# Kernel optimization log

Measured on AMD Instinct MI355X. Metric: run time of the kernel, lower is better.

The kernel has to match this reference:

```python
import jax, jax.numpy as jnp
import numpy as np

B, T, H = 1, 1024, 1024
F2, F3 = 2 * H, 3 * H          # routed / shared ffn dims
S, E, K, R = 8, 32, 4, 64      # shared experts, routed experts, top-k, router rank
EPS = 1e-6


def _rms(x, w):
    # RMSNorm: x * rsqrt(mean(x^2) + eps) * weight
    return x * jax.lax.rsqrt(jnp.mean(x * x, axis=-1, keepdims=True) + EPS) * w


def setup_inputs() -> dict:
    key = jax.random.key(0)
    ks = jax.random.split(key, 10)
    s = 0.02
    return {
        "x": jax.random.normal(ks[0], (B, T, H), dtype=jnp.float32),
        "sn": jnp.ones((S, H), dtype=jnp.float32),                       # shared RMSNorm weights
        "sw1": jax.random.normal(ks[1], (S, H, F3), dtype=jnp.float32) * s,
        "sw2": jax.random.normal(ks[2], (S, F3, H), dtype=jnp.float32) * s,
        "sw3": jax.random.normal(ks[3], (S, H, F3), dtype=jnp.float32) * s,
        "rw1": jax.random.normal(ks[4], (E, H, F2), dtype=jnp.float32) * s,
        "rw2": jax.random.normal(ks[5], (E, F2, H), dtype=jnp.float32) * s,
        "rw3": jax.random.normal(ks[6], (E, H, F2), dtype=jnp.float32) * s,
        "rd": jax.random.normal(ks[7], (H, R), dtype=jnp.float32) * s,   # router_down
        "ru": jax.random.normal(ks[8], (R, E), dtype=jnp.float32) * s,   # router_up
    }


def reference(x, sn, sw1, sw2, sw3, rw1, rw2, rw3, rd, ru):
    b, t, h = x.shape
    xf = x.reshape(-1, h)                                   # [Tk, H]

    # ---- shared experts (AdvancedExpert: RMSNorm + SwiGLU + residual), averaged ----
    xn = _rms(xf[None], sn[:, None, :])                     # [S, Tk, H]
    g = jax.nn.silu(jnp.einsum('sth,shf->stf', xn, sw1))
    v = jnp.einsum('sth,shf->stf', xn, sw3)
    ff = jnp.einsum('stf,sfh->sth', g * v, sw2)             # [S, Tk, H]
    shared = jnp.mean(ff, axis=0) + xf                      # residual averages to +xf

    # ---- router: low-rank logits, top-k, softmax over selected ----
    logits = (xf @ rd) @ ru                                 # [Tk, E]
    rweights, sel = jax.lax.top_k(logits, K)                # [Tk, K]
    rweights = jax.nn.softmax(rweights, axis=-1)
    onehot = jax.nn.one_hot(sel, E, dtype=xf.dtype)         # [Tk, K, E]
    combine = jnp.einsum('tk,tke->te', rweights, onehot)    # [Tk, E]

    # ---- routed experts (Expert: SwiGLU, no norm/residual), weighted combine ----
    g = jax.nn.silu(jnp.einsum('th,ehf->etf', xf, rw1))     # [E, Tk, F2]
    v = jnp.einsum('th,ehf->etf', xf, rw3)
    eouts = jnp.einsum('etf,efh->eth', g * v, rw2)          # [E, Tk, H]
    routed = jnp.einsum('eth,te->th', eouts, combine)

    out = (shared + routed).reshape(b, t, h)

    # ---- aux: load-balance loss = variance (unbiased, like torch .var()) of expert counts ----
    counts = jnp.sum(jax.nn.one_hot(sel.reshape(-1), E, dtype=jnp.float32), axis=0)
    load_balance_loss = jnp.var(counts, ddof=1)
    return out, load_balance_loss
```

## Files before the change

### kernel.cpp

```cpp
#include <hip/hip_runtime.h>
#include <hip/hip_bf16.h>
#include <math.h>

#define TK 1024
#define HD 1024
#define NF3 3072
#define NF2 2048
#define NSH 8
#define NEX 32
#define KSEL 4
#define RRK 64

typedef short bf16x8 __attribute__((ext_vector_type(8)));
typedef float f32x4 __attribute__((ext_vector_type(4)));
typedef unsigned short u16;

__device__ __forceinline__ u16 f2b(float f){
  union{float f; unsigned u;} c; c.f=f;
  unsigned r = c.u + 0x7FFFu + ((c.u>>16)&1u);
  return (u16)(r>>16);
}

__device__ __forceinline__ unsigned pk2(float a, float b){
  __hip_bfloat162 h = __float22bfloat162_rn(float2{a, b});
  union{__hip_bfloat162 h; unsigned u;} c; c.h = h; return c.u;
}

__device__ __forceinline__ int swz8(int row, int c){
  return row*128 + ((c ^ (row&7))<<4);
}

__device__ __forceinline__ int scrofs(int k, int nq){
  return k*256 + (((nq&8) | ((nq&7)^(k&7)))<<4);
}
__device__ __forceinline__ int chunkperm(int c, int k){
  return (c&8) | ((c&7)^(k&7));
}

#define GLDS16(gptr, lptr) \
  __builtin_amdgcn_global_load_lds((const __attribute__((address_space(1))) unsigned*)(gptr), \
                                   (__attribute__((address_space(3))) unsigned*)(lptr), 16, 0, 0)


__global__ void init_kernel(int* counts, int* cursors){
  int i = threadIdx.x;
  if (i < NEX){ counts[i]=0; cursors[i]=0; }
}

__global__ void rms_kernel(const float* __restrict__ x, const float* __restrict__ sn,
                           u16* __restrict__ xb, u16* __restrict__ xnb,
                           float* __restrict__ out, float* __restrict__ rvec, int writeXnb)
{
  const int t = blockIdx.x, tid = threadIdx.x;
  const float4 v = ((const float4*)(x + (size_t)t*HD))[tid];
  float ss = v.x*v.x + v.y*v.y + v.z*v.z + v.w*v.w;
  #pragma unroll
  for (int m=32;m>=1;m>>=1) ss += __shfl_xor(ss, m);
  __shared__ float red[4];
  if ((tid&63)==0) red[tid>>6]=ss;
  __syncthreads();
  const float r = rsqrtf((red[0]+red[1]+red[2]+red[3])*(1.0f/HD) + 1e-6f);
  if (tid==0) rvec[t] = r;
  ushort4 o; o.x=f2b(v.x); o.y=f2b(v.y); o.z=f2b(v.z); o.w=f2b(v.w);
  ((ushort4*)(xb + (size_t)t*HD))[tid] = o;
  if (writeXnb){
    ((float4*)(out + (size_t)t*HD))[tid] = v;
    #pragma unroll
    for (int s=0;s<NSH;s++){
      const float4 g = ((const float4*)(sn + (size_t)s*HD))[tid];
      ushort4 q;
      q.x=f2b(v.x*r*g.x); q.y=f2b(v.y*r*g.y); q.z=f2b(v.z*r*g.z); q.w=f2b(v.w*r*g.w);
      ((ushort4*)(xnb + ((size_t)s*TK + t)*HD))[tid] = q;
    }
  }
}

__global__ void router_kernel(const float* __restrict__ x, const float* __restrict__ rd,
                              const float* __restrict__ ru,
                              int* __restrict__ sel, float* __restrict__ wts,
                              int* __restrict__ counts)
{
  const int t = blockIdx.x, l = threadIdx.x;
  __shared__ float xl[HD];
  __shared__ float xr[RRK];
  __shared__ float lg[NEX];
  const float* xrow = x + (size_t)t*HD;
  for (int i=l;i<HD;i+=64) xl[i]=xrow[i];
  __syncthreads();
  float acc=0.f;
  for (int h=0;h<HD;h++) acc += xl[h]*rd[h*RRK + l];
  xr[l]=acc;
  __syncthreads();
  if (l < NEX){
    float a=0.f;
    for (int r=0;r<RRK;r++) a += xr[r]*ru[r*NEX + l];
    lg[l]=a;
  }
  __syncthreads();
  if (l==0){
    int   sk[KSEL]; float val[KSEL]; unsigned used=0;
    for (int k=0;k<KSEL;k++){
      float best=-1e30f; int bi=0;
      for (int e=0;e<NEX;e++){
        if (used & (1u<<e)) continue;
        if (lg[e] > best){ best=lg[e]; bi=e; }
      }
      used |= (1u<<bi); sk[k]=bi; val[k]=best;
    }
    const float m = val[0];
    float w[KSEL], s=0.f;
    for (int k=0;k<KSEL;k++){ w[k]=expf(val[k]-m); s+=w[k]; }
    for (int k=0;k<KSEL;k++){
      sel[t*KSEL+k]=sk[k]; wts[t*KSEL+k]=w[k]/s;
      atomicAdd(&counts[sk[k]], 1);
    }
  }
}

__global__ void scan_loss_kernel(const int* __restrict__ counts, int* __restrict__ offsets,
                                 float* __restrict__ out_loss)
{
  if (threadIdx.x==0){
    int off=0; float var=0.f;
    for (int e=0;e<NEX;e++){
      offsets[e]=off; off+=counts[e];
      float d = (float)counts[e] - 128.0f;
      var += d*d;
    }
    out_loss[0] = var * (1.0f/31.0f);
  }
}

__global__ void scatter_kernel(const int* __restrict__ sel, const float* __restrict__ wts,
                               const int* __restrict__ offsets, int* __restrict__ cursors,
                               int* __restrict__ tok_of, float* __restrict__ wt_of,
                               int* __restrict__ slot_of)
{
  const int id = blockIdx.x*256 + threadIdx.x;
  const int e = sel[id];
  const int pos = atomicAdd(&cursors[e], 1);
  const int slot = offsets[e] + pos;
  tok_of[slot] = id >> 2;
  wt_of[slot]  = wts[id];
  slot_of[id]  = slot;
}

template<bool SN>
__global__ __launch_bounds__(256) void convT_kernel(const float* __restrict__ src,
                                                    u16* __restrict__ dst, int K, int N,
                                                    const float* __restrict__ sn)
{
  const int z = blockIdx.z;
  const int n0 = blockIdx.x*64, k0 = blockIdx.y*64;
  src += (size_t)z*K*N; dst += (size_t)z*N*K;
  const float* snp = SN ? (sn + (size_t)z*HD + k0) : nullptr;
  __shared__ float tile[64][65];
  const int t = threadIdx.x;
  const int kr = t>>4, nc = t&15;
  #pragma unroll
  for (int i=0;i<4;i++){
    const int k = kr + 16*i;
    const float4 v = *(const float4*)(src + (size_t)(k0+k)*N + n0 + nc*4);
    tile[k][nc*4+0]=v.x; tile[k][nc*4+1]=v.y; tile[k][nc*4+2]=v.z; tile[k][nc*4+3]=v.w;
  }
  __syncthreads();
  const int nr = t>>3, kc = t&7;
  float sv[8];
  #pragma unroll
  for (int j=0;j<8;j++) sv[j] = SN ? snp[kc*8+j] : 1.0f;
  #pragma unroll
  for (int p=0;p<2;p++){
    const int n = nr + 32*p;
    unsigned d0 = pk2(tile[kc*8+0][n]*sv[0], tile[kc*8+1][n]*sv[1]);
    unsigned d1 = pk2(tile[kc*8+2][n]*sv[2], tile[kc*8+3][n]*sv[3]);
    unsigned d2 = pk2(tile[kc*8+4][n]*sv[4], tile[kc*8+5][n]*sv[5]);
    unsigned d3 = pk2(tile[kc*8+6][n]*sv[6], tile[kc*8+7][n]*sv[7]);
    *(uint4*)(dst + (size_t)(n0+n)*K + k0 + kc*8) = make_uint4(d0,d1,d2,d3);
  }
}

__global__ __launch_bounds__(256, 2) void up2_kernel(
    const u16* __restrict__ xb, const u16* __restrict__ W1t, const u16* __restrict__ W3t,
    u16* __restrict__ Ob, const float* __restrict__ rvec)
{
  const int b = blockIdx.x;
  const int z = b & 7;
  const int r = b >> 3;
  const int xt = r >> 2;
  const int yt = r & 3;
  const int m0 = yt * 256;
  const int n0 = xt * 64;
  const u16* W1 = W1t + (size_t)z*NF3*HD;
  const u16* W3 = W3t + (size_t)z*NF3*HD;
  u16* O = Ob + (size_t)z*TK*NF3;

  __shared__ alignas(16) u16 Al[256*64];
  __shared__ alignas(16) u16 Bl[128*64];
  char* Alc = (char*)Al; char* Blc = (char*)Bl;

  const int tid = threadIdx.x, w = tid>>6, l = tid&63;
  const int wm = (w>>1)*128, wn = (w&1)*32;

  const u16 *asrc[8], *bsrc[4];
  #pragma unroll
  for (int p=0;p<8;p++){
    const int id = p*256 + tid;
    const int row = id>>3;
    const int chunk = (id&7) ^ (row&7);
    asrc[p] = xb + (size_t)(m0+row)*HD + chunk*8;
  }
  #pragma unroll
  for (int p=0;p<4;p++){
    const int id = p*256 + tid;
    const int row = id>>3;
    const int chunk = (id&7) ^ (row&7);
    bsrc[p] = ((row<64) ? (W1 + (size_t)(n0+row)*HD) : (W3 + (size_t)(n0+row-64)*HD)) + chunk*8;
  }

  f32x4 acc1[8][2] = {}; f32x4 acc3[8][2] = {};

  auto issue = [&](int ke){
    #pragma unroll
    for (int p=0;p<8;p++) GLDS16(asrc[p] + ke, Alc + ((p*256+tid)<<4));
    #pragma unroll
    for (int p=0;p<4;p++) GLDS16(bsrc[p] + ke, Blc + ((p*256+tid)<<4));
  };
  auto compute = [&](){
    #pragma unroll
    for (int kh=0;kh<2;kh++){
      bf16x8 af[8], b1[2], b3[2];
      #pragma unroll
      for (int mi=0;mi<8;mi++)
        af[mi] = *(const bf16x8*)(Alc + swz8(wm + mi*16 + (l&15), kh*4 + (l>>4)));
      #pragma unroll
      for (int ni=0;ni<2;ni++){
        b1[ni] = *(const bf16x8*)(Blc + swz8(     wn + ni*16 + (l&15), kh*4 + (l>>4)));
        b3[ni] = *(const bf16x8*)(Blc + swz8(64 + wn + ni*16 + (l&15), kh*4 + (l>>4)));
      }
      #pragma unroll
      for (int mi=0;mi<8;mi++){
        #pragma unroll
        for (int ni=0;ni<2;ni++){
          acc1[mi][ni] = __builtin_amdgcn_mfma_f32_16x16x32_bf16(af[mi], b1[ni], acc1[mi][ni], 0,0,0);
          acc3[mi][ni] = __builtin_amdgcn_mfma_f32_16x16x32_bf16(af[mi], b3[ni], acc3[mi][ni], 0,0,0);
        }
      }
    }
  };

  constexpr int NT = HD/64;
  for (int t=0; t<NT; ++t){
    issue(t*64);
    __syncthreads();
    compute();
    __syncthreads();
  }

  #pragma unroll
  for (int mi=0;mi<8;mi++){
    #pragma unroll
    for (int ni=0;ni<2;ni++){
      #pragma unroll
      for (int r2=0;r2<4;r2++){
        const int row = wm + mi*16 + ((l>>4)<<2) + r2;
        const float rr = rvec[m0+row];
        const float v1 = rr*acc1[mi][ni][r2], v3 = rr*acc3[mi][ni][r2];
        const float h = v3 * v1 / (1.0f + expf(-v1));
        O[(size_t)(m0+row)*NF3 + n0 + wn + ni*16 + (l&15)] = f2b(h);
      }
    }
  }
}

__global__ __launch_bounds__(256, 2) void sdown_kernel(
    const u16* __restrict__ Hb, const u16* __restrict__ W2t, float* __restrict__ Sbuf)
{
  const int b = blockIdx.x;
  const int e = b & 7;
  const int r = b >> 3;
  const int xt = r >> 3;
  const int yt = r & 7;
  const int m0 = yt * 128;
  const int n0 = xt * 128;
  const u16* A  = Hb  + (size_t)e*TK*NF3;
  const u16* W2 = W2t + (size_t)e*HD*NF3;

  __shared__ alignas(16) u16 Al[128*64];
  __shared__ alignas(16) u16 Bl[128*64];
  char* Alc = (char*)Al; char* Blc = (char*)Bl;

  const int tid = threadIdx.x, w = tid>>6, l = tid&63;
  const int wm = (w>>1)*64, wn = (w&1)*64;

  const u16 *asrc[4], *bsrc[4];
  #pragma unroll
  for (int p=0;p<4;p++){
    const int id = p*256 + tid;
    const int row = id>>3;
    const int chunk = (id&7)^(row&7);
    asrc[p] = A  + (size_t)(m0+row)*NF3 + chunk*8;
    bsrc[p] = W2 + (size_t)(n0+row)*NF3 + chunk*8;
  }

  f32x4 acc[4][4] = {};

  auto issue = [&](int ke){
    #pragma unroll
    for (int p=0;p<4;p++) GLDS16(asrc[p] + ke, Alc + ((p*256+tid)<<4));
    #pragma unroll
    for (int p=0;p<4;p++) GLDS16(bsrc[p] + ke, Blc + ((p*256+tid)<<4));
  };
  auto compute = [&](){
    #pragma unroll
    for (int kh=0;kh<2;kh++){
      bf16x8 af[4], bfr[4];
      #pragma unroll
      for (int mi=0;mi<4;mi++)
        af[mi]  = *(const bf16x8*)(Alc + swz8(wm + mi*16 + (l&15), kh*4 + (l>>4)));
      #pragma unroll
      for (int ni=0;ni<4;ni++)
        bfr[ni] = *(const bf16x8*)(Blc + swz8(wn + ni*16 + (l&15), kh*4 + (l>>4)));
      #pragma unroll
      for (int mi=0;mi<4;mi++){
        #pragma unroll
        for (int ni=0;ni<4;ni++)
          acc[mi][ni] = __builtin_amdgcn_mfma_f32_16x16x32_bf16(af[mi], bfr[ni], acc[mi][ni], 0,0,0);
      }
    }
  };

  constexpr int NT = NF3/64;
  for (int t=0; t<NT; ++t){
    issue(t*64);
    __syncthreads();
    compute();
    __syncthreads();
  }

  #pragma unroll
  for (int mi=0;mi<4;mi++){
    #pragma unroll
    for (int ni=0;ni<4;ni++){
      #pragma unroll
      for (int r2=0;r2<4;r2++){
        const int row = wm + mi*16 + ((l>>4)<<2) + r2;
        const int col = n0 + wn + ni*16 + (l&15);
        Sbuf[((size_t)e*TK + m0+row)*HD + col] = acc[mi][ni][r2];
      }
    }
  }
}

__global__ __launch_bounds__(256, 2) void up3_kernel(
    const u16* __restrict__ xb, const float* __restrict__ W1b, const float* __restrict__ W3b,
    u16* __restrict__ Ob, const int* __restrict__ counts, const int* __restrict__ offsets,
    const int* __restrict__ tok_of)
{
  const int z  = blockIdx.z;
  const int m0 = blockIdx.y * 256;
  const int n0 = blockIdx.x * 64;
  const int Meff = counts[z];
  if (m0 >= Meff) return;
  const int off = offsets[z];
  const int* toks = tok_of + off;
  const float* W1 = W1b + (size_t)z*HD*NF2;
  const float* W3 = W3b + (size_t)z*HD*NF2;
  u16* O = Ob + (size_t)off*NF2;

  __shared__ alignas(16) u16   Al[256*64];
  __shared__ alignas(16) float Scr[2*64*64];
  __shared__ alignas(16) u16   Bl[2*64*64];
  char* Alc = (char*)Al; char* Blc = (char*)Bl; char* Scc = (char*)Scr;

  const int tid = threadIdx.x, w = tid>>6, l = tid&63;
  const int wm = (w>>1)*128, wn = (w&1)*32;

  int aofs[8];
  #pragma unroll
  for (int p=0;p<8;p++){
    const int id = p*256 + tid;
    const int row = id>>3;
    const int chunk = (id&7) ^ (row&7);
    int mg = m0 + row;
    mg = toks[(mg < Meff) ? mg : (Meff-1)];
    aofs[p] = mg*HD + chunk*8;
  }
  int bofs[8];
  #pragma unroll
  for (int p=0;p<8;p++){
    const int id = (p&3)*256 + tid;
    const int k = id>>4, c = id&15;
    bofs[p] = k*NF2 + n0 + chunkperm(c, k)*4;
  }

  f32x4 acc1[8][2] = {}; f32x4 acc3[8][2] = {};

  constexpr int NT = HD/64;
  for (int t=0; t<NT; ++t){
    #pragma unroll
    for (int p=0;p<8;p++) GLDS16(xb + aofs[p] + t*64, Alc + ((p*256+tid)<<4));
    #pragma unroll
    for (int p=0;p<4;p++) GLDS16(W1 + bofs[p] + (size_t)t*64*NF2, Scc + ((p*256+tid)<<4));
    #pragma unroll
    for (int p=4;p<8;p++) GLDS16(W3 + bofs[p] + (size_t)t*64*NF2, Scc + 16384 + (((p-4)*256+tid)<<4));
    __syncthreads();

    {
      const int nq = tid&15, kq = tid>>4;
      #pragma unroll
      for (int m2=0;m2<2;m2++){
        const char* sc = Scc + m2*16384;
        char* bd = Blc + m2*8192;
        float4 v[4];
        #pragma unroll
        for (int i=0;i<4;i++) v[i] = *(const float4*)(sc + scrofs(kq*4+i, nq));
        #pragma unroll
        for (int j=0;j<4;j++){
          const int n = nq*4+j;
          uint2 wv;
          wv.x = pk2(v[0][j], v[1][j]);
          wv.y = pk2(v[2][j], v[3][j]);
          *(uint2*)(bd + n*128 + (((kq>>1)^(n&7))<<4) + ((kq&1)<<3)) = wv;
        }
      }
    }
    __syncthreads();

    #pragma unroll
    for (int kh=0;kh<2;kh++){
      bf16x8 af[8], b1[2], b3[2];
      #pragma unroll
      for (int mi=0;mi<8;mi++)
        af[mi] = *(const bf16x8*)(Alc + swz8(wm + mi*16 + (l&15), kh*4 + (l>>4)));
      #pragma unroll
      for (int ni=0;ni<2;ni++){
        b1[ni] = *(const bf16x8*)(Blc +        swz8(wn + ni*16 + (l&15), kh*4 + (l>>4)));
        b3[ni] = *(const bf16x8*)(Blc + 8192 + swz8(wn + ni*16 + (l&15), kh*4 + (l>>4)));
      }
      #pragma unroll
      for (int mi=0;mi<8;mi++){
        #pragma unroll
        for (int ni=0;ni<2;ni++){
          acc1[mi][ni] = __builtin_amdgcn_mfma_f32_16x16x32_bf16(af[mi], b1[ni], acc1[mi][ni], 0,0,0);
          acc3[mi][ni] = __builtin_amdgcn_mfma_f32_16x16x32_bf16(af[mi], b3[ni], acc3[mi][ni], 0,0,0);
        }
      }
    }
    __syncthreads();
  }

  #pragma unroll
  for (int mi=0;mi<8;mi++){
    #pragma unroll
    for (int ni=0;ni<2;ni++){
      #pragma unroll
      for (int r2=0;r2<4;r2++){
        const int row = wm + mi*16 + ((l>>4)<<2) + r2;
        const int mg  = m0 + row;
        if (mg >= Meff) continue;
        const float v1 = acc1[mi][ni][r2], v3 = acc3[mi][ni][r2];
        const float h = v3 * v1 / (1.0f + expf(-v1));
        O[(size_t)mg*NF2 + n0 + wn + ni*16 + (l&15)] = f2b(h);
      }
    }
  }
}

__global__ __launch_bounds__(256, 2) void rdown_f_kernel(
    const u16* __restrict__ Gb, const float* __restrict__ W2b, float* __restrict__ Ebuf,
    const int* __restrict__ counts, const int* __restrict__ offsets)
{
  const int z  = blockIdx.z;
  const int m0 = blockIdx.y * 128;
  const int n0 = blockIdx.x * 64;
  const int Meff = counts[z];
  if (m0 >= Meff) return;
  const int off = offsets[z];
  const u16* A = Gb + (size_t)off*NF2;
  const float* W2 = W2b + (size_t)z*NF2*HD;

  __shared__ alignas(16) u16   Al[128*64];
  __shared__ alignas(16) float Scr[64*64];
  __shared__ alignas(16) u16   Bl[64*64];
  char* Alc = (char*)Al; char* Blc = (char*)Bl; char* Scc = (char*)Scr;

  const int tid = threadIdx.x, w = tid>>6, l = tid&63;
  const int wm = (w>>1)*64, wn = (w&1)*32;

  int aofs[4];
  #pragma unroll
  for (int p=0;p<4;p++){
    const int id = p*256 + tid;
    const int row = id>>3;
    const int chunk = (id&7) ^ (row&7);
    int mg = m0 + row; if (mg >= Meff) mg = Meff-1;
    aofs[p] = mg*NF2 + chunk*8;
  }
  int bofs[4];
  #pragma unroll
  for (int p=0;p<4;p++){
    const int id = p*256 + tid;
    const int k = id>>4, c = id&15;
    bofs[p] = k*HD + n0 + chunkperm(c, k)*4;
  }

  f32x4 acc[4][2] = {};

  constexpr int NT = NF2/64;
  for (int t=0; t<NT; ++t){
    #pragma unroll
    for (int p=0;p<4;p++) GLDS16(A + aofs[p] + t*64, Alc + ((p*256+tid)<<4));
    #pragma unroll
    for (int p=0;p<4;p++) GLDS16(W2 + bofs[p] + (size_t)t*64*HD, Scc + ((p*256+tid)<<4));
    __syncthreads();

    {
      const int nq = tid&15, kq = tid>>4;
      float4 v[4];
      #pragma unroll
      for (int i=0;i<4;i++) v[i] = *(const float4*)(Scc + scrofs(kq*4+i, nq));
      #pragma unroll
      for (int j=0;j<4;j++){
        const int n = nq*4+j;
        uint2 wv;
        wv.x = pk2(v[0][j], v[1][j]);
        wv.y = pk2(v[2][j], v[3][j]);
        *(uint2*)(Blc + n*128 + (((kq>>1)^(n&7))<<4) + ((kq&1)<<3)) = wv;
      }
    }
    __syncthreads();

    #pragma unroll
    for (int kh=0;kh<2;kh++){
      bf16x8 af[4], bfr[2];
      #pragma unroll
      for (int mi=0;mi<4;mi++)
        af[mi]  = *(const bf16x8*)(Alc + swz8(wm + mi*16 + (l&15), kh*4 + (l>>4)));
      #pragma unroll
      for (int ni=0;ni<2;ni++)
        bfr[ni] = *(const bf16x8*)(Blc + swz8(wn + ni*16 + (l&15), kh*4 + (l>>4)));
      #pragma unroll
      for (int mi=0;mi<4;mi++){
        #pragma unroll
        for (int ni=0;ni<2;ni++)
          acc[mi][ni] = __builtin_amdgcn_mfma_f32_16x16x32_bf16(af[mi], bfr[ni], acc[mi][ni], 0,0,0);
      }
    }
    __syncthreads();
  }

  #pragma unroll
  for (int mi=0;mi<4;mi++){
    #pragma unroll
    for (int ni=0;ni<2;ni++){
      #pragma unroll
      for (int r2=0;r2<4;r2++){
        const int row = wm + mi*16 + ((l>>4)<<2) + r2;
        const int mg  = m0 + row;
        if (mg >= Meff) continue;
        const int col = n0 + wn + ni*16 + (l&15);
        Ebuf[((size_t)off+mg)*HD + col] = acc[mi][ni][r2];
      }
    }
  }
}

__global__ __launch_bounds__(256) void combine_kernel(
    const float* __restrict__ x, const float* __restrict__ Sbuf,
    const float* __restrict__ Ebuf, const float* __restrict__ wts,
    const int* __restrict__ slot_of, float* __restrict__ out)
{
  const int t = blockIdx.x, tid = threadIdx.x;
  float4 o = ((const float4*)(x + (size_t)t*HD))[tid];
  float4 s = make_float4(0.f,0.f,0.f,0.f);
  #pragma unroll
  for (int e=0;e<NSH;e++){
    const float4 v = ((const float4*)(Sbuf + ((size_t)e*TK + t)*HD))[tid];
    s.x+=v.x; s.y+=v.y; s.z+=v.z; s.w+=v.w;
  }
  o.x += 0.125f*s.x; o.y += 0.125f*s.y; o.z += 0.125f*s.z; o.w += 0.125f*s.w;
  #pragma unroll
  for (int k=0;k<KSEL;k++){
    const float wgt = wts[t*KSEL+k];
    const int slot  = slot_of[t*KSEL+k];
    const float4 v = ((const float4*)(Ebuf + (size_t)slot*HD))[tid];
    o.x += wgt*v.x; o.y += wgt*v.y; o.z += wgt*v.z; o.w += wgt*v.w;
  }
  ((float4*)(out + (size_t)t*HD))[tid] = o;
}


template<int NDIM, bool ROUTED>
__global__ __launch_bounds__(256, 2) void up_kernel(
    const u16* __restrict__ Ab, const float* __restrict__ W1b, const float* __restrict__ W3b,
    u16* __restrict__ Ob, const int* __restrict__ counts, const int* __restrict__ offsets,
    const int* __restrict__ tok_of)
{
  const int z  = blockIdx.z;
  const int m0 = blockIdx.y * 128;
  const int n0 = blockIdx.x * 64;

  int Meff; const u16* A; const float *W1, *W3; u16* O; const int* toks = nullptr;
  if (ROUTED){
    Meff = counts[z];
    if (m0 >= Meff) return;
    const int off = offsets[z];
    toks = tok_of + off; A = Ab;
    W1 = W1b + (size_t)z*HD*NDIM; W3 = W3b + (size_t)z*HD*NDIM;
    O  = Ob  + (size_t)off*NDIM;
  } else {
    Meff = TK;
    A  = Ab  + (size_t)z*TK*HD;
    W1 = W1b + (size_t)z*HD*NDIM; W3 = W3b + (size_t)z*HD*NDIM;
    O  = Ob  + (size_t)z*TK*NDIM;
  }

  __shared__ alignas(16) u16 Al[128*64];
  __shared__ alignas(16) u16 Bl[128*64];
  char* Alc = (char*)Al; char* Blc = (char*)Bl;

  const int tid = threadIdx.x, w = tid>>6, l = tid&63;
  const int wm = (w>>1)*64, wn = (w&1)*32;

  const u16* asrc[4];
  #pragma unroll
  for (int p=0;p<4;p++){
    const int id  = p*256 + tid;
    const int row = id>>3;
    const int chunk = (id&7) ^ (row&7);
    int mg = m0 + row;
    if (ROUTED) mg = toks[(mg < Meff) ? mg : (Meff-1)];
    asrc[p] = A + (size_t)mg*HD + chunk*8;
  }
  const int br = tid&127, bhalf = tid>>7;
  const float* bsrc0 = ((br<64) ? W1 : W3) + (size_t)bhalf*32*NDIM + (n0 + (br&63));

  f32x4 acc1[4][2] = {}; f32x4 acc3[4][2] = {};

  auto issueA = [&](int ke){
    #pragma unroll
    for (int p=0;p<4;p++) GLDS16(asrc[p] + ke, Alc + ((p*256+tid)<<4));
  };
  auto loadB = [&](float* f, int t){
    const float* s_ = bsrc0 + (size_t)t*64*NDIM;
    #pragma unroll
    for (int i=0;i<32;i++) f[i] = s_[(size_t)i*NDIM];
  };
  auto writeB = [&](const float* f){
    #pragma unroll
    for (int j=0;j<4;j++){
      const uint4 v = make_uint4(pk2(f[j*8+0],f[j*8+1]), pk2(f[j*8+2],f[j*8+3]),
                                 pk2(f[j*8+4],f[j*8+5]), pk2(f[j*8+6],f[j*8+7]));
      *(uint4*)(Blc + swz8(br, bhalf*4+j)) = v;
    }
  };
  auto compute = [&](){
    #pragma unroll
    for (int kh=0;kh<2;kh++){
      bf16x8 af[4], b1[2], b3[2];
      #pragma unroll
      for (int mi=0;mi<4;mi++)
        af[mi] = *(const bf16x8*)(Alc + swz8(wm + mi*16 + (l&15), kh*4 + (l>>4)));
      #pragma unroll
      for (int ni=0;ni<2;ni++){
        b1[ni] = *(const bf16x8*)(Blc + swz8(     wn + ni*16 + (l&15), kh*4 + (l>>4)));
        b3[ni] = *(const bf16x8*)(Blc + swz8(64 + wn + ni*16 + (l&15), kh*4 + (l>>4)));
      }
      #pragma unroll
      for (int mi=0;mi<4;mi++){
        #pragma unroll
        for (int ni=0;ni<2;ni++){
          acc1[mi][ni] = __builtin_amdgcn_mfma_f32_16x16x32_bf16(af[mi], b1[ni], acc1[mi][ni], 0,0,0);
          acc3[mi][ni] = __builtin_amdgcn_mfma_f32_16x16x32_bf16(af[mi], b3[ni], acc3[mi][ni], 0,0,0);
        }
      }
    }
  };

  float fb[32];
  loadB(fb, 0);
  constexpr int NT = HD/64;
  for (int t=0; t<NT; ++t){
    writeB(fb);
    issueA(t*64);
    __syncthreads();
    if (t+1 < NT) loadB(fb, t+1);
    compute();
    __syncthreads();
  }

  #pragma unroll
  for (int mi=0;mi<4;mi++){
    #pragma unroll
    for (int ni=0;ni<2;ni++){
      #pragma unroll
      for (int r2=0;r2<4;r2++){
        const int row = wm + mi*16 + ((l>>4)<<2) + r2;
        const int mg  = m0 + row;
        if (ROUTED && mg >= Meff) continue;
        const float v1 = acc1[mi][ni][r2], v3 = acc3[mi][ni][r2];
        const float h = v3 * v1 / (1.0f + expf(-v1));
        O[(size_t)mg*NDIM + n0 + wn + ni*16 + (l&15)] = f2b(h);
      }
    }
  }
}

template<bool ROUTED>
__global__ __launch_bounds__(256, 2) void down_kernel(
    const u16* __restrict__ Ab, const float* __restrict__ W2b, float* __restrict__ out,
    const int* __restrict__ counts, const int* __restrict__ offsets,
    const int* __restrict__ tok_of, const float* __restrict__ wt_of)
{
  const int z  = blockIdx.z;
  const int m0 = blockIdx.y * 128;
  const int n0 = blockIdx.x * 128;
  constexpr int KT  = ROUTED ? NF2 : NF3;
  constexpr int KCH = ROUTED ? 512 : 1024;

  int Meff = TK, off = 0, e, kb;
  const u16* A; const float* W2;
  if (ROUTED){
    e = z>>2; kb = (z&3)*KCH;
    Meff = counts[e];
    if (m0 >= Meff) return;
    off = offsets[e];
    A  = Ab  + (size_t)off*NF2;
    W2 = W2b + (size_t)e*NF2*HD;
  } else {
    e = z/3; kb = (z - e*3)*KCH;
    A  = Ab  + (size_t)e*TK*NF3;
    W2 = W2b + (size_t)e*NF3*HD;
  }

  __shared__ alignas(16) u16 Al[128*64];
  __shared__ alignas(16) u16 Bl[128*64];
  char* Alc = (char*)Al; char* Blc = (char*)Bl;

  const int tid = threadIdx.x, w = tid>>6, l = tid&63;
  const int wm = (w>>1)*64, wn = (w&1)*64;

  const u16* asrc[4];
  #pragma unroll
  for (int p=0;p<4;p++){
    const int id  = p*256 + tid;
    const int row = id>>3;
    const int chunk = (id&7) ^ (row&7);
    int mg = m0 + row;
    if (ROUTED && mg >= Meff) mg = Meff-1;
    asrc[p] = A + (size_t)mg*KT + kb + chunk*8;
  }
  const int br = tid&127, bhalf = tid>>7;
  const float* bsrc0 = W2 + (size_t)(bhalf*32 + kb)*HD + (n0 + br);

  f32x4 acc[4][4] = {};

  auto issueA = [&](int ke){
    #pragma unroll
    for (int p=0;p<4;p++) GLDS16(asrc[p] + ke, Alc + ((p*256+tid)<<4));
  };
  auto loadB = [&](float* f, int t){
    const float* s_ = bsrc0 + (size_t)t*64*HD;
    #pragma unroll
    for (int i=0;i<32;i++) f[i] = s_[(size_t)i*HD];
  };
  auto writeB = [&](const float* f){
    #pragma unroll
    for (int j=0;j<4;j++){
      const uint4 v = make_uint4(pk2(f[j*8+0],f[j*8+1]), pk2(f[j*8+2],f[j*8+3]),
                                 pk2(f[j*8+4],f[j*8+5]), pk2(f[j*8+6],f[j*8+7]));
      *(uint4*)(Blc + swz8(br, bhalf*4+j)) = v;
    }
  };
  auto compute = [&](){
    #pragma unroll
    for (int kh=0;kh<2;kh++){
      bf16x8 af[4], bfr[4];
      #pragma unroll
      for (int mi=0;mi<4;mi++)
        af[mi]  = *(const bf16x8*)(Alc + swz8(wm + mi*16 + (l&15), kh*4 + (l>>4)));
      #pragma unroll
      for (int ni=0;ni<4;ni++)
        bfr[ni] = *(const bf16x8*)(Blc + swz8(wn + ni*16 + (l&15), kh*4 + (l>>4)));
      #pragma unroll
      for (int mi=0;mi<4;mi++){
        #pragma unroll
        for (int ni=0;ni<4;ni++)
          acc[mi][ni] = __builtin_amdgcn_mfma_f32_16x16x32_bf16(af[mi], bfr[ni], acc[mi][ni], 0,0,0);
      }
    }
  };

  float fb[32];
  loadB(fb, 0);
  constexpr int NT = KCH/64;
  for (int t=0; t<NT; ++t){
    writeB(fb);
    issueA(t*64);
    __syncthreads();
    if (t+1 < NT) loadB(fb, t+1);
    compute();
    __syncthreads();
  }

  #pragma unroll
  for (int mi=0;mi<4;mi++){
    #pragma unroll
    for (int ni=0;ni<4;ni++){
      #pragma unroll
      for (int r2=0;r2<4;r2++){
        const int row = wm + mi*16 + ((l>>4)<<2) + r2;
        const int mg  = m0 + row;
        const int col = n0 + wn + ni*16 + (l&15);
        if (ROUTED){
          if (mg >= Meff) continue;
          const int slot = off + mg;
          atomicAdd(&out[(size_t)tok_of[slot]*HD + col], wt_of[slot]*acc[mi][ni][r2]);
        } else {
          atomicAdd(&out[(size_t)mg*HD + col], 0.125f*acc[mi][ni][r2]);
        }
      }
    }
  }
}


extern "C" void kernel_launch(void* const* d_in, const int* in_sizes, int n_in,
                              void* d_out, int out_size, void* d_ws, size_t ws_size,
                              hipStream_t stream)
{
  const float* x   = (const float*)d_in[0];
  const float* sn  = (const float*)d_in[1];
  const float* sw1 = (const float*)d_in[2];
  const float* sw2 = (const float*)d_in[3];
  const float* sw3 = (const float*)d_in[4];
  const float* rw1 = (const float*)d_in[5];
  const float* rw2 = (const float*)d_in[6];
  const float* rw3 = (const float*)d_in[7];
  const float* rd  = (const float*)d_in[8];
  const float* ru  = (const float*)d_in[9];
  float* out = (float*)d_out;

  char* ws = (char*)d_ws;
  u16* xb    = (u16*)(ws);
  u16* xnb   = (u16*)(ws + ((size_t)2<<20));
  u16* Hbuf  = (u16*)(ws + ((size_t)18<<20));
  u16* Gbuf  = (u16*)(ws + ((size_t)66<<20));
  char* aux  = ws + ((size_t)82<<20);
  int*   sel    = (int*)(aux);
  float* wts    = (float*)(aux + 16384);
  int*   counts = (int*)(aux + 32768);
  int*   offs   = (int*)(aux + 33024);
  int*   curs   = (int*)(aux + 33280);
  int*   tok_of = (int*)(aux + 34816);
  float* wt_of  = (float*)(aux + 34816 + 16384);
  int*   slot_of= (int*)(aux + 34816 + 32768);
  float* rvec   = (float*)(aux + 34816 + 49152);
  const size_t WSLICE   = (size_t)NSH*NF3*HD*2;
  const size_t WBASE    = (size_t)84<<20;
  const size_t SBUF_OFF = WBASE + 3*WSLICE;
  const size_t SBUF_SZ  = (size_t)NSH*TK*HD*4;
  const size_t EBUF_OFF = SBUF_OFF + SBUF_SZ;
  const size_t EBUF_SZ  = (size_t)TK*KSEL*HD*4;
  const bool  full = ws_size >= EBUF_OFF + EBUF_SZ;
  u16* sw1t = (u16*)(ws + WBASE);
  u16* sw3t = (u16*)(ws + WBASE + WSLICE);
  u16* sw2t = (u16*)(ws + WBASE + 2*WSLICE);
  float* Sbuf = (float*)(ws + SBUF_OFF);
  float* Ebuf = (float*)(ws + EBUF_OFF);

  hipLaunchKernelGGL(init_kernel, dim3(1), dim3(64), 0, stream, counts, curs);
  hipLaunchKernelGGL(rms_kernel, dim3(TK), dim3(256), 0, stream, x, sn, xb, xnb, out, rvec,
                     full ? 0 : 1);
  hipLaunchKernelGGL(router_kernel, dim3(TK), dim3(64), 0, stream, x, rd, ru, sel, wts, counts);
  hipLaunchKernelGGL(scan_loss_kernel, dim3(1), dim3(64), 0, stream, counts, offs,
                     out + (size_t)TK*HD);
  hipLaunchKernelGGL(scatter_kernel, dim3(16), dim3(256), 0, stream, sel, wts, offs, curs,
                     tok_of, wt_of, slot_of);

  if (full){
    hipLaunchKernelGGL((convT_kernel<true>),  dim3(NF3/64, HD/64, NSH), dim3(256), 0, stream,
                       sw1, sw1t, HD, NF3, sn);
    hipLaunchKernelGGL((convT_kernel<true>),  dim3(NF3/64, HD/64, NSH), dim3(256), 0, stream,
                       sw3, sw3t, HD, NF3, sn);
    hipLaunchKernelGGL((convT_kernel<false>), dim3(HD/64, NF3/64, NSH), dim3(256), 0, stream,
                       sw2, sw2t, NF3, HD, nullptr);
    hipLaunchKernelGGL(up2_kernel, dim3((NF3/64)*(TK/256)*NSH), dim3(256), 0, stream,
                       xb, sw1t, sw3t, Hbuf, rvec);
    hipLaunchKernelGGL(up3_kernel, dim3(NF2/64, 2, NEX), dim3(256), 0, stream,
                       xb, rw1, rw3, Gbuf, counts, offs, tok_of);
    hipLaunchKernelGGL(sdown_kernel, dim3((HD/128)*(TK/128)*NSH), dim3(256), 0, stream,
                       Hbuf, sw2t, Sbuf);
    hipLaunchKernelGGL(rdown_f_kernel, dim3(HD/64, 2, NEX), dim3(256), 0, stream,
                       Gbuf, rw2, Ebuf, counts, offs);
    hipLaunchKernelGGL(combine_kernel, dim3(TK), dim3(256), 0, stream,
                       x, Sbuf, Ebuf, wts, slot_of, out);
  } else {
    hipLaunchKernelGGL((up_kernel<NF3, false>), dim3(NF3/64, TK/128, NSH), dim3(256), 0,
                       stream, xnb, sw1, sw3, Hbuf, nullptr, nullptr, nullptr);
    hipLaunchKernelGGL((up_kernel<NF2, true>), dim3(NF2/64, TK/128, NEX), dim3(256), 0,
                       stream, xb, rw1, rw3, Gbuf, counts, offs, tok_of);
    hipLaunchKernelGGL((down_kernel<false>), dim3(HD/128, TK/128, NSH*3), dim3(256), 0, stream,
                       Hbuf, sw2, out, nullptr, nullptr, nullptr, nullptr);
    hipLaunchKernelGGL((down_kernel<true>), dim3(HD/128, TK/128, NEX*4), dim3(256), 0, stream,
                       Gbuf, rw2, out, counts, offs, tok_of, wt_of);
  }
}
```

Before: 598.7 us.

## Fuse shared-expert weight transpose and bf16 conversion into up-projection GEMM

Removes the two separate convT passes for sw1/sw3 and has the up-projection kernel load fp32 weight tiles directly into LDS scratch. There it scales them by the RMSNorm weights, converts to bf16 and writes a swizzled transposed B tile before the MFMA loop. This saves a full read and write of the shared weights through global memory, plus two launches. In exchange each block re-reads fp32 weights for every M tile (4x redundancy across M blocks), LDS use grows and an extra sync is added per K step. Helpers chunkperm and scrofs are referenced but not shown.

```diff
diff --git a/kernel.cpp b/kernel.cpp
--- a/kernel.cpp
+++ b/kernel.cpp
@@ -179,9 +179,9 @@
   }
 }
 
-__global__ __launch_bounds__(256, 2) void up2_kernel(
-    const u16* __restrict__ xb, const u16* __restrict__ W1t, const u16* __restrict__ W3t,
-    u16* __restrict__ Ob, const float* __restrict__ rvec)
+__global__ __launch_bounds__(256, 2) void up2f_kernel(
+    const u16* __restrict__ xb, const float* __restrict__ W1b, const float* __restrict__ W3b,
+    const float* __restrict__ snb, u16* __restrict__ Ob, const float* __restrict__ rvec)
 {
   const int b = blockIdx.x;
   const int z = b & 7;
@@ -190,42 +190,74 @@
   const int yt = r & 3;
   const int m0 = yt * 256;
   const int n0 = xt * 64;
-  const u16* W1 = W1t + (size_t)z*NF3*HD;
-  const u16* W3 = W3t + (size_t)z*NF3*HD;
+  const float* W1 = W1b + (size_t)z*HD*NF3;
+  const float* W3 = W3b + (size_t)z*HD*NF3;
+  const float* sn = snb + (size_t)z*HD;
   u16* O = Ob + (size_t)z*TK*NF3;
 
-  __shared__ alignas(16) u16 Al[256*64];
-  __shared__ alignas(16) u16 Bl[128*64];
-  char* Alc = (char*)Al; char* Blc = (char*)Bl;
+  __shared__ alignas(16) u16   Al[256*64];
+  __shared__ alignas(16) float Scr[2*64*64];
+  __shared__ alignas(16) u16   Bl[2*64*64];
+  char* Alc = (char*)Al; char* Blc = (char*)Bl; char* Scc = (char*)Scr;
 
   const int tid = threadIdx.x, w = tid>>6, l = tid&63;
   const int wm = (w>>1)*128, wn = (w&1)*32;
 
-  const u16 *asrc[8], *bsrc[4];
+  int aofs[8];
   #pragma unroll
   for (int p=0;p<8;p++){
     const int id = p*256 + tid;
     const int row = id>>3;
     const int chunk = (id&7) ^ (row&7);
-    asrc[p] = xb + (size_t)(m0+row)*HD + chunk*8;
-  }
-  #pragma unroll
-  for (int p=0;p<4;p++){
-    const int id = p*256 + tid;
-    const int row = id>>3;
-    const int chunk = (id&7) ^ (row&7);
-    bsrc[p] = ((row<64) ? (W1 + (size_t)(n0+row)*HD) : (W3 + (size_t)(n0+row-64)*HD)) + chunk*8;
+    aofs[p] = (m0+row)*HD + chunk*8;
+  }
+  int bofs[8];
+  #pragma unroll
+  for (int p=0;p<8;p++){
+    const int id = (p&3)*256 + tid;
+    const int k = id>>4, c = id&15;
+    bofs[p] = k*NF3 + n0 + chunkperm(c, k)*4;
   }
 
   f32x4 acc1[8][2] = {}; f32x4 acc3[8][2] = {};
 
-  auto issue = [&](int ke){
-    #pragma unroll
-    for (int p=0;p<8;p++) GLDS16(asrc[p] + ke, Alc + ((p*256+tid)<<4));
-    #pragma unroll
-    for (int p=0;p<4;p++) GLDS16(bsrc[p] + ke, Blc + ((p*256+tid)<<4));
-  };
-  auto compute = [&](){
+  constexpr int NT = HD/64;
+  for (int t=0; t<NT; ++t){
+    #pragma unroll
+    for (int p=0;p<8;p++) GLDS16(xb + aofs[p] + t*64, Alc + ((p*256+tid)<<4));
+    #pragma unroll
+    for (int p=0;p<4;p++) GLDS16(W1 + bofs[p] + (size_t)t*64*NF3, Scc + ((p*256+tid)<<4));
+    #pragma unroll
+    for (int p=4;p<8;p++) GLDS16(W3 + bofs[p] + (size_t)t*64*NF3, Scc + 16384 + (((p-4)*256+tid)<<4));
+    __syncthreads();
+
+    {
+      const int nq = tid&15, kq = tid>>4;
+      float sv[4];
+      #pragma unroll
+      for (int i=0;i<4;i++) sv[i] = sn[t*64 + kq*4 + i];
+      #pragma unroll
+      for (int m2=0;m2<2;m2++){
+        const char* sc = Scc + m2*16384;
+        char* bd = Blc + m2*8192;
+        float4 v[4];
+        #pragma unroll
+        for (int i=0;i<4;i++){
+          v[i] = *(const float4*)(sc + scrofs(kq*4+i, nq));
+          v[i].x *= sv[i]; v[i].y *= sv[i]; v[i].z *= sv[i]; v[i].w *= sv[i];
+        }
+        #pragma unroll
+        for (int j=0;j<4;j++){
+          const int n = nq*4+j;
+          uint2 wv;
+          wv.x = pk2(v[0][j], v[1][j]);
+          wv.y = pk2(v[2][j], v[3][j]);
+          *(uint2*)(bd + n*128 + (((kq>>1)^(n&7))<<4) + ((kq&1)<<3)) = wv;
+        }
+      }
+    }
+    __syncthreads();
+
     #pragma unroll
     for (int kh=0;kh<2;kh++){
       bf16x8 af[8], b1[2], b3[2];
@@ -234,8 +266,8 @@
         af[mi] = *(const bf16x8*)(Alc + swz8(wm + mi*16 + (l&15), kh*4 + (l>>4)));
       #pragma unroll
       for (int ni=0;ni<2;ni++){
-        b1[ni] = *(const bf16x8*)(Blc + swz8(     wn + ni*16 + (l&15), kh*4 + (l>>4)));
-        b3[ni] = *(const bf16x8*)(Blc + swz8(64 + wn + ni*16 + (l&15), kh*4 + (l>>4)));
+        b1[ni] = *(const bf16x8*)(Blc +        swz8(wn + ni*16 + (l&15), kh*4 + (l>>4)));
+        b3[ni] = *(const bf16x8*)(Blc + 8192 + swz8(wn + ni*16 + (l&15), kh*4 + (l>>4)));
       }
       #pragma unroll
       for (int mi=0;mi<8;mi++){
@@ -246,13 +278,6 @@
         }
       }
     }
-  };
-
-  constexpr int NT = HD/64;
-  for (int t=0; t<NT; ++t){
-    issue(t*64);
-    __syncthreads();
-    compute();
     __syncthreads();
   }
 
@@ -863,8 +888,6 @@
   const size_t EBUF_OFF = SBUF_OFF + SBUF_SZ;
   const size_t EBUF_SZ  = (size_t)TK*KSEL*HD*4;
   const bool  full = ws_size >= EBUF_OFF + EBUF_SZ;
-  u16* sw1t = (u16*)(ws + WBASE);
-  u16* sw3t = (u16*)(ws + WBASE + WSLICE);
   u16* sw2t = (u16*)(ws + WBASE + 2*WSLICE);
   float* Sbuf = (float*)(ws + SBUF_OFF);
   float* Ebuf = (float*)(ws + EBUF_OFF);
@@ -879,14 +902,10 @@
                      tok_of, wt_of, slot_of);
 
   if (full){
-    hipLaunchKernelGGL((convT_kernel<true>),  dim3(NF3/64, HD/64, NSH), dim3(256), 0, stream,
-                       sw1, sw1t, HD, NF3, sn);
-    hipLaunchKernelGGL((convT_kernel<true>),  dim3(NF3/64, HD/64, NSH), dim3(256), 0, stream,
-                       sw3, sw3t, HD, NF3, sn);
     hipLaunchKernelGGL((convT_kernel<false>), dim3(HD/64, NF3/64, NSH), dim3(256), 0, stream,
                        sw2, sw2t, NF3, HD, nullptr);
-    hipLaunchKernelGGL(up2_kernel, dim3((NF3/64)*(TK/256)*NSH), dim3(256), 0, stream,
-                       xb, sw1t, sw3t, Hbuf, rvec);
+    hipLaunchKernelGGL(up2f_kernel, dim3((NF3/64)*(TK/256)*NSH), dim3(256), 0, stream,
+                       xb, sw1, sw3, sn, Hbuf, rvec);
     hipLaunchKernelGGL(up3_kernel, dim3(NF2/64, 2, NEX), dim3(256), 0, stream,
                        xb, rw1, rw3, Gbuf, counts, offs, tok_of);
     hipLaunchKernelGGL(sdown_kernel, dim3((HD/128)*(TK/128)*NSH), dim3(256), 0, stream,
```

Measured after the change: 625.3 us. 1.04x slower.
